# Optimization experiments

Measured on AMD Instinct MI355X. Metric: run time of the kernel, lower is better.

The kernel has to match this reference:

```python
import jax, jax.numpy as jnp
import numpy as np
import math

V, D, L, FF, H, DH, W, DM, T, B = 32000, 1024, 4, 4096, 16, 64, 256, 64, 1024, 1


def rms_norm(x, w):
    return x * jax.lax.rsqrt(jnp.mean(x * x, axis=-1, keepdims=True) + 1e-6) * w


def setup_inputs() -> dict:
    key = jax.random.key(0)
    ks = jax.random.split(key, 16)
    s = 0.02
    return {
        "x": jax.random.randint(ks[0], (B, T), 0, V),
        "embed": jax.random.normal(ks[1], (V, D), jnp.float32) * s,
        "ln_in_w": jnp.ones((D,), jnp.float32),
        "ln1_w": jnp.ones((L, D), jnp.float32),
        "lnd_w": jnp.ones((L, D), jnp.float32),
        "qkv_w": jax.random.normal(ks[2], (L, 3 * H * DH, D), jnp.float32) * s,
        "swa_out_w": jax.random.normal(ks[3], (L, D, H * DH), jnp.float32) * s,
        "k_w": jax.random.normal(ks[4], (L, H * DM, D), jnp.float32) * s,
        "v_w": jax.random.normal(ks[5], (L, H * DM, D), jnp.float32) * s,
        "q_w": jax.random.normal(ks[6], (L, H * DM, D), jnp.float32) * s,
        "beta_w": jax.random.normal(ks[7], (L, H, D), jnp.float32) * s,
        "mem_out_w": jax.random.normal(ks[8], (L, D, H * DM), jnp.float32) * s,
        "gate_w": jax.random.normal(ks[9], (L, D, D), jnp.float32) * s,
        "comb_w": jax.random.normal(ks[10], (L, D, D), jnp.float32) * s,
        "ln2_w": jnp.ones((L, D), jnp.float32),
        "wg": jax.random.normal(ks[11], (L, FF, D), jnp.float32) * s,
        "wu": jax.random.normal(ks[12], (L, FF, D), jnp.float32) * s,
        "wo": jax.random.normal(ks[13], (L, D, FF), jnp.float32) * s,
        "ln_out_w": jnp.ones((D,), jnp.float32),
    }


def _swa(h1, qkv_w, out_w):
    # h1: [B,T,D]
    qkv = jnp.einsum('btd,ed->bte', h1, qkv_w)  # [B,T,3*H*DH]
    q, k, v = jnp.split(qkv, 3, axis=-1)
    q = q.reshape(h1.shape[0], T, H, DH).transpose(0, 2, 1, 3)
    k = k.reshape(h1.shape[0], T, H, DH).transpose(0, 2, 1, 3)
    v = v.reshape(h1.shape[0], T, H, DH).transpose(0, 2, 1, 3)
    scores = jnp.einsum('bhqd,bhkd->bhqk', q, k) * (DH ** -0.5)
    pos = jnp.arange(T)
    dist = pos[:, None] - pos[None, :]
    allowed = (dist >= 0) & (dist < W)  # causal sliding window
    scores = jnp.where(allowed[None, None], scores, -jnp.inf)
    attn = jax.nn.softmax(scores, axis=-1)
    out = jnp.einsum('bhqk,bhkd->bhqd', attn, v)
    out = out.transpose(0, 2, 1, 3).reshape(h1.shape[0], T, H * DH)
    return jnp.einsum('bte,de->btd', out, out_w)


def _delta(h2, k_w, v_w, q_w, beta_w, mem_out_w):
    Bv = h2.shape[0]
    proj = lambda w: jnp.einsum('btd,ed->bte', h2, w).reshape(Bv, T, H, DM).transpose(0, 2, 1, 3)
    keys, values, queries = proj(k_w), proj(v_w), proj(q_w)
    beta = jax.nn.sigmoid(jnp.einsum('btd,hd->bht', h2, beta_w))  # [B,H,T]
    keys = keys / jnp.maximum(jnp.linalg.norm(keys, axis=-1, keepdims=True), 1e-12)
    queries = queries / jnp.maximum(jnp.linalg.norm(queries, axis=-1, keepdims=True), 1e-12)
    log_retain = jnp.log(1.0 - beta + 1e-8)
    cum_log = jnp.cumsum(log_retain, axis=-1)  # [B,H,T]
    log_decay = cum_log[..., :, None] - cum_log[..., None, :]  # [B,H,T,T]
    causal = jnp.triu(jnp.ones((T, T), dtype=bool))  # matches torch.triu mask in source
    decay = jnp.exp(jnp.minimum(log_decay, 0.0)) * causal
    kq = jnp.einsum('bhid,bhjd->bhij', queries, keys) / math.sqrt(DM)
    weights = kq * decay
    out = jnp.einsum('bhij,bhjd->bhid', weights, values)
    out = out + beta[..., None] * values
    out = out.transpose(0, 2, 1, 3).reshape(Bv, T, H * DM)
    return jnp.einsum('bte,de->btd', out, mem_out_w)


def reference(x, embed, ln_in_w, ln1_w, lnd_w, qkv_w, swa_out_w, k_w, v_w, q_w,
              beta_w, mem_out_w, gate_w, comb_w, ln2_w, wg, wu, wo, ln_out_w):
    h = rms_norm(embed[x], ln_in_w)  # [B,T,D]
    for l in range(L):
        h1 = rms_norm(h, ln1_w[l])
        h2 = rms_norm(h, lnd_w[l])
        local = _swa(h1, qkv_w[l], swa_out_w[l])
        global_ctx = _delta(h2, k_w[l], v_w[l], q_w[l], beta_w[l], mem_out_w[l])
        gate = jax.nn.sigmoid(jnp.einsum('btd,ed->bte', h1, gate_w[l]))
        mixed = jnp.einsum('btd,ed->bte', gate * local + (1.0 - gate) * global_ctx, comb_w[l])
        h = h + mixed
        hn = rms_norm(h, ln2_w[l])
        ffn = jnp.einsum('btf,df->btd', jax.nn.silu(jnp.einsum('btd,fd->btf', hn, wg[l])) * jnp.einsum('btd,fd->btf', hn, wu[l]), wo[l])
        h = h + ffn
    logits = jnp.einsum('btd,vd->btv', rms_norm(h, ln_out_w), embed)  # tied head
    return logits
```

## Files before the change

### kernel.cpp

```cpp
#include <hip/hip_runtime.h>

typedef unsigned short u16;
typedef unsigned int   u32;
typedef __attribute__((ext_vector_type(8))) __bf16 bfv8;
typedef __attribute__((ext_vector_type(4))) float  f32x4;

__device__ __forceinline__ u16 f2bf(float f){
  u32 u = __builtin_bit_cast(u32, f);
  return (u16)((u + 0x7FFFu + ((u >> 16) & 1u)) >> 16);
}
__device__ __forceinline__ float bf2f(u16 b){
  return __builtin_bit_cast(float, ((u32)b) << 16);
}
__device__ __forceinline__ u32 pk2(float a, float b){
  return (u32)f2bf(a) | ((u32)f2bf(b) << 16);
}
__device__ __forceinline__ float wsum(float v){
  #pragma unroll
  for (int m = 32; m > 0; m >>= 1) v += __shfl_xor(v, m, 64);
  return v;
}
__device__ __forceinline__ void gload16(const void* g, void* l){
  __builtin_amdgcn_global_load_lds((const __attribute__((address_space(1))) void*)g,
                                   (__attribute__((address_space(3))) void*)l, 16, 0, 0);
}

struct CBatch { const float* s[12]; long long p4[13]; u16* dst; };
__global__ __launch_bounds__(256) void flm_conv(CBatch cb)
{
  const int seg = blockIdx.y;
  const long long base = cb.p4[seg];
  const long long n4 = cb.p4[seg + 1] - base;
  const float* __restrict__ src = cb.s[seg];
  uint2* __restrict__ dst = (uint2*)cb.dst + base;
  for (long long i = (long long)blockIdx.x * 256 + threadIdx.x; i < n4;
       i += (long long)gridDim.x * 256){
    float4 v = ((const float4*)src)[i];
    uint2 p; p.x = pk2(v.x, v.y); p.y = pk2(v.z, v.w);
    dst[i] = p;
  }
}

struct GDesc {
  const u16* A; const float* Bw; float* Cf; u16* Cb;
  int lda, ldb, ldc, kbeg, kend, blk0, epi, pad;
};
struct GBatch { GDesc d[6]; int ng, total; };

template<bool BW>
__global__ __launch_bounds__(512) void flm_mgemm(GBatch gb)
{
  constexpr int LDK = BW ? 64 : 72;
  __shared__ u16 sA[128][LDK];
  __shared__ u16 sB[128][LDK];
  const int tid = threadIdx.x, lane = tid & 63, w = tid >> 6;

  const int T = gb.total, bid = blockIdx.x;
  const int q8 = T >> 3, r8 = T & 7, xc = bid & 7, of = bid >> 3;
  const int lin = (xc < r8 ? xc * (q8 + 1) : r8 * (q8 + 1) + (xc - r8) * q8) + of;
  int di = 0;
  #pragma unroll
  for (int i = 1; i < 6; i++) if (i < gb.ng && lin >= gb.d[i].blk0) di = i;
  const GDesc g = gb.d[di];
  const int local = lin - g.blk0;
  const int row0 = (local & 7) * 128;
  const int col0 = (local >> 3) * 128;
  const int wr = (w >> 2) * 64, wc = (w & 3) * 32;

  f32x4 acc[4][2];
  #pragma unroll
  for (int m = 0; m < 4; m++)
    #pragma unroll
    for (int n = 0; n < 2; n++)
      acc[m][n] = (f32x4){0.f, 0.f, 0.f, 0.f};

  const int csw = ((lane & 7) ^ (lane >> 3)) * 8;
  const u16* B16 = (const u16*)g.Bw;

  for (int k0 = g.kbeg; k0 < g.kend; k0 += 64){
    if constexpr (BW){
      const u16* a0 = g.A + (size_t)(row0 + w*16 + (lane>>3)) * g.lda + k0 + csw;
      const u16* b0 = B16 + (size_t)(col0 + w*16 + (lane>>3)) * g.ldb + k0 + csw;
      gload16(a0,                     &sA[w*16    ][0]);
      gload16(a0 + (size_t)8*g.lda,   &sA[w*16 + 8][0]);
      gload16(b0,                     &sB[w*16    ][0]);
      gload16(b0 + (size_t)8*g.ldb,   &sB[w*16 + 8][0]);
    } else {
      #pragma unroll
      for (int i = 0; i < 2; i++){
        int idx = tid + i * 512;
        int r = idx >> 3, c = (idx & 7) * 8;
        *(uint4*)&sA[r][c] = *(const uint4*)(g.A + (size_t)(row0 + r) * g.lda + k0 + c);
      }
      #pragma unroll
      for (int i = 0; i < 4; i++){
        int idx = tid + i * 512;
        int r = idx >> 4, c = (idx & 15) * 4;
        float4 v = *(const float4*)(g.Bw + (size_t)(col0 + r) * g.ldb + k0 + c);
        uint2 p; p.x = pk2(v.x, v.y); p.y = pk2(v.z, v.w);
        *(uint2*)&sB[r][c] = p;
      }
    }
    __syncthreads();
    #pragma unroll
    for (int kk = 0; kk < 2; kk++){
      bfv8 af[4], bfr[2];
      #pragma unroll
      for (int m = 0; m < 4; m++){
        int row = wr + m*16 + (lane & 15);
        if constexpr (BW){
          int slot = (kk*4 + (lane >> 4)) ^ (row & 7);
          af[m] = *(const bfv8*)((const char*)sA + row*128 + slot*16);
        } else {
          af[m] = *(const bfv8*)&sA[row][kk*32 + (lane >> 4) * 8];
        }
      }
      #pragma unroll
      for (int n = 0; n < 2; n++){
        int row = wc + n*16 + (lane & 15);
        if constexpr (BW){
          int slot = (kk*4 + (lane >> 4)) ^ (row & 7);
          bfr[n] = *(const bfv8*)((const char*)sB + row*128 + slot*16);
        } else {
          bfr[n] = *(const bfv8*)&sB[row][kk*32 + (lane >> 4) * 8];
        }
      }
      #pragma unroll
      for (int m = 0; m < 4; m++)
        #pragma unroll
        for (int n = 0; n < 2; n++)
          acc[m][n] = __builtin_amdgcn_mfma_f32_16x16x32_bf16(af[m], bfr[n], acc[m][n], 0, 0, 0);
    }
    __syncthreads();
  }

  #pragma unroll
  for (int m = 0; m < 4; m++){
    int rbase = row0 + wr + m*16 + (lane >> 4) * 4;
    #pragma unroll
    for (int n = 0; n < 2; n++){
      int col = col0 + wc + n*16 + (lane & 15);
      #pragma unroll
      for (int j = 0; j < 4; j++){
        float v = acc[m][n][j];
        size_t o = (size_t)(rbase + j) * g.ldc + col;
        switch (g.epi){
          case 0: g.Cf[o] = v; break;
          case 1: g.Cb[o] = f2bf(v); break;
          default: atomicAdd(&g.Cf[o], v); break;
        }
      }
    }
  }
}

__global__ __launch_bounds__(256) void flm_mix(
    const float* __restrict__ gr, const float* __restrict__ lo,
    const float* __restrict__ gl, u16* __restrict__ o)
{
  int i = blockIdx.x * 256 + threadIdx.x;
  float4 gv = ((const float4*)gr)[i];
  float4 lv = ((const float4*)lo)[i];
  float4 bv = ((const float4*)gl)[i];
  float sx = 1.f/(1.f+expf(-gv.x)), sy = 1.f/(1.f+expf(-gv.y));
  float sz = 1.f/(1.f+expf(-gv.z)), sw = 1.f/(1.f+expf(-gv.w));
  uint2 p;
  p.x = pk2(sx*lv.x + (1.f-sx)*bv.x, sy*lv.y + (1.f-sy)*bv.y);
  p.y = pk2(sz*lv.z + (1.f-sz)*bv.z, sw*lv.w + (1.f-sw)*bv.w);
  ((uint2*)o)[i] = p;
}

__global__ __launch_bounds__(256) void flm_silu(
    const u16* __restrict__ gg, const u16* __restrict__ uu, u16* __restrict__ o)
{
  int i = blockIdx.x * 256 + threadIdx.x;
  uint2 gv = ((const uint2*)gg)[i];
  uint2 uv = ((const uint2*)uu)[i];
  float g0 = bf2f((u16)gv.x), g1 = bf2f((u16)(gv.x >> 16));
  float g2 = bf2f((u16)gv.y), g3 = bf2f((u16)(gv.y >> 16));
  float u0 = bf2f((u16)uv.x), u1 = bf2f((u16)(uv.x >> 16));
  float u2 = bf2f((u16)uv.y), u3 = bf2f((u16)(uv.y >> 16));
  float a = g0 / (1.f + expf(-g0)) * u0;
  float b = g1 / (1.f + expf(-g1)) * u1;
  float c = g2 / (1.f + expf(-g2)) * u2;
  float d = g3 / (1.f + expf(-g3)) * u3;
  uint2 p; p.x = pk2(a, b); p.y = pk2(c, d);
  ((uint2*)o)[i] = p;
}

__global__ __launch_bounds__(256) void flm_embed(
    const int* __restrict__ x, const float* __restrict__ embed,
    const float* __restrict__ w, float* __restrict__ h)
{
  int t = blockIdx.x, tid = threadIdx.x;
  int tok = x[t];
  float4 v = ((const float4*)(embed + (size_t)tok * 1024))[tid];
  float ss = v.x*v.x + v.y*v.y + v.z*v.z + v.w*v.w;
  ss = wsum(ss);
  __shared__ float red[4];
  if ((tid & 63) == 0) red[tid >> 6] = ss;
  __syncthreads();
  float inv = rsqrtf((red[0]+red[1]+red[2]+red[3]) * (1.f/1024.f) + 1e-6f);
  float4 wv = ((const float4*)w)[tid];
  float4 o; o.x = v.x*inv*wv.x; o.y = v.y*inv*wv.y; o.z = v.z*inv*wv.z; o.w = v.w*inv*wv.w;
  ((float4*)(h + (size_t)t * 1024))[tid] = o;
}

__global__ __launch_bounds__(256) void flm_rms(
    const float* __restrict__ h, const float* __restrict__ w1, const float* __restrict__ w2,
    u16* __restrict__ o1, u16* __restrict__ o2)
{
  int t = blockIdx.x, tid = threadIdx.x;
  float4 v = ((const float4*)(h + (size_t)t * 1024))[tid];
  float ss = v.x*v.x + v.y*v.y + v.z*v.z + v.w*v.w;
  ss = wsum(ss);
  __shared__ float red[4];
  if ((tid & 63) == 0) red[tid >> 6] = ss;
  __syncthreads();
  float inv = rsqrtf((red[0]+red[1]+red[2]+red[3]) * (1.f/1024.f) + 1e-6f);
  {
    float4 wv = ((const float4*)w1)[tid];
    uint2 p; p.x = pk2(v.x*inv*wv.x, v.y*inv*wv.y); p.y = pk2(v.z*inv*wv.z, v.w*inv*wv.w);
    ((uint2*)(o1 + (size_t)t * 1024))[tid] = p;
  }
  if (o2 != nullptr){
    float4 wv = ((const float4*)w2)[tid];
    uint2 p; p.x = pk2(v.x*inv*wv.x, v.y*inv*wv.y); p.y = pk2(v.z*inv*wv.z, v.w*inv*wv.w);
    ((uint2*)(o2 + (size_t)t * 1024))[tid] = p;
  }
}

__global__ __launch_bounds__(64) void flm_betanorm(
    const u16* __restrict__ h2, const float* __restrict__ bw, float* __restrict__ beta,
    u16* __restrict__ keys, u16* __restrict__ queries)
{
  int t = blockIdx.x, lane = threadIdx.x;
  float hv[16];
  #pragma unroll
  for (int i = 0; i < 16; i++) hv[i] = bf2f(h2[(size_t)t*1024 + i*64 + lane]);
  for (int h = 0; h < 16; h++){
    float p = 0.f;
    #pragma unroll
    for (int i = 0; i < 16; i++) p += hv[i] * bw[h*1024 + i*64 + lane];
    p = wsum(p);
    if (lane == 0) beta[t*16 + h] = 1.f / (1.f + expf(-p));
  }
  #pragma unroll
  for (int h = 0; h < 16; h++){
    size_t idx = (size_t)t * 1024 + h * 64 + lane;
    float v = bf2f(keys[idx]);
    float nrm = fmaxf(sqrtf(wsum(v * v)), 1e-12f);
    keys[idx] = f2bf(v / nrm);
    float q = bf2f(queries[idx]);
    float qn = fmaxf(sqrtf(wsum(q * q)), 1e-12f);
    queries[idx] = f2bf(q / qn);
  }
}

__global__ __launch_bounds__(256) void flm_attn(
    const u16* __restrict__ qkv,
    const u16* __restrict__ keys, const u16* __restrict__ values, const u16* __restrict__ queries,
    const float* __restrict__ beta, u16* __restrict__ aout, u16* __restrict__ dout)
{
  __shared__ u16 sK[64][72];
  __shared__ u16 sVt[64][72];
  __shared__ u16 sP[4][16][72];
  const int tid = threadIdx.x, lane = tid & 63, w = tid >> 6;
  const int qt = blockIdx.x, h = blockIdx.y;
  const int base = h * 64;
  const int ri = w*16 + (lane>>4)*4;

  if (blockIdx.z == 0){
    bfv8 aq[2];
    {
      int qrow = qt*64 + w*16 + (lane & 15);
      #pragma unroll
      for (int kk = 0; kk < 2; kk++)
        aq[kk] = *(const bfv8*)(qkv + (size_t)qrow*3072 + base + kk*32 + (lane>>4)*8);
    }
    f32x4 acc_o[4];
    float m_r[4], l_r[4];
    #pragma unroll
    for (int n = 0; n < 4; n++) acc_o[n] = (f32x4){0.f,0.f,0.f,0.f};
    #pragma unroll
    for (int r = 0; r < 4; r++){ m_r[r] = -1e30f; l_r[r] = 0.f; }
    const int jt0 = (qt >= 4) ? qt - 4 : 0;

    for (int jt = qt; jt >= jt0; jt--){
      #pragma unroll
      for (int i = 0; i < 2; i++){
        int idx = tid + i*256;
        int r = idx >> 3, c = (idx & 7) * 8;
        uint4 kv = *(const uint4*)(qkv + (size_t)(jt*64+r)*3072 + 1024 + base + c);
        *(uint4*)&sK[r][c] = kv;
        uint4 vv = *(const uint4*)(qkv + (size_t)(jt*64+r)*3072 + 2048 + base + c);
        u16 tmp[8]; *(uint4*)tmp = vv;
        #pragma unroll
        for (int e = 0; e < 8; e++) sVt[c+e][r] = tmp[e];
      }
      __syncthreads();

      f32x4 sv[4];
      #pragma unroll
      for (int n = 0; n < 4; n++) sv[n] = (f32x4){0.f,0.f,0.f,0.f};
      #pragma unroll
      for (int kk = 0; kk < 2; kk++){
        #pragma unroll
        for (int n = 0; n < 4; n++){
          bfv8 bk = *(const bfv8*)&sK[n*16 + (lane & 15)][(lane>>4)*8 + kk*32];
          sv[n] = __builtin_amdgcn_mfma_f32_16x16x32_bf16(aq[kk], bk, sv[n], 0, 0, 0);
        }
      }
      #pragma unroll
      for (int n = 0; n < 4; n++){
        int cj = n*16 + (lane & 15);
        #pragma unroll
        for (int r = 0; r < 4; r++){
          float s = sv[n][r] * 0.125f;
          if (jt == qt)      { if (cj > ri + r) s = -1e30f; }
          else if (jt == jt0 && qt - jt0 == 4) { if (cj <= ri + r) s = -1e30f; }
          sv[n][r] = s;
        }
      }
      float pv[4][4], scl[4];
      #pragma unroll
      for (int r = 0; r < 4; r++){
        float mx = -1e30f;
        #pragma unroll
        for (int n = 0; n < 4; n++) mx = fmaxf(mx, sv[n][r]);
        #pragma unroll
        for (int m = 1; m < 16; m <<= 1) mx = fmaxf(mx, __shfl_xor(mx, m, 64));
        float mn = fmaxf(m_r[r], mx);
        float sc = expf(m_r[r] - mn);
        m_r[r] = mn; scl[r] = sc;
        float rs = 0.f;
        #pragma unroll
        for (int n = 0; n < 4; n++){ float p = expf(sv[n][r] - mn); pv[n][r] = p; rs += p; }
        #pragma unroll
        for (int m = 1; m < 16; m <<= 1) rs += __shfl_xor(rs, m, 64);
        l_r[r] = l_r[r] * sc + rs;
      }
      #pragma unroll
      for (int n = 0; n < 4; n++){
        #pragma unroll
        for (int r = 0; r < 4; r++){
          acc_o[n][r] *= scl[r];
          sP[w][(lane>>4)*4 + r][n*16 + (lane & 15)] = f2bf(pv[n][r]);
        }
      }
      #pragma unroll
      for (int kk = 0; kk < 2; kk++){
        bfv8 ap = *(const bfv8*)&sP[w][lane & 15][(lane>>4)*8 + kk*32];
        #pragma unroll
        for (int n = 0; n < 4; n++){
          bfv8 bv = *(const bfv8*)&sVt[n*16 + (lane & 15)][(lane>>4)*8 + kk*32];
          acc_o[n] = __builtin_amdgcn_mfma_f32_16x16x32_bf16(ap, bv, acc_o[n], 0, 0, 0);
        }
      }
      __syncthreads();
    }

    #pragma unroll
    for (int n = 0; n < 4; n++){
      int col = base + n*16 + (lane & 15);
      #pragma unroll
      for (int r = 0; r < 4; r++){
        int row = qt*64 + ri + r;
        aout[(size_t)row*1024 + col] = f2bf(acc_o[n][r] / l_r[r]);
      }
    }
  } else {
    bfv8 aq[2];
    {
      int qrow = qt*64 + w*16 + (lane & 15);
      #pragma unroll
      for (int kk = 0; kk < 2; kk++)
        aq[kk] = *(const bfv8*)(queries + (size_t)qrow*1024 + base + kk*32 + (lane>>4)*8);
    }
    f32x4 acc_o[4];
    #pragma unroll
    for (int n = 0; n < 4; n++) acc_o[n] = (f32x4){0.f,0.f,0.f,0.f};

    for (int jt = qt; jt < 16; jt++){
      #pragma unroll
      for (int i = 0; i < 2; i++){
        int idx = tid + i*256;
        int r = idx >> 3, c = (idx & 7) * 8;
        uint4 kv = *(const uint4*)(keys + (size_t)(jt*64+r)*1024 + base + c);
        *(uint4*)&sK[r][c] = kv;
        uint4 vv = *(const uint4*)(values + (size_t)(jt*64+r)*1024 + base + c);
        u16 tmp[8]; *(uint4*)tmp = vv;
        #pragma unroll
        for (int e = 0; e < 8; e++) sVt[c+e][r] = tmp[e];
      }
      __syncthreads();

      f32x4 sv[4];
      #pragma unroll
      for (int n = 0; n < 4; n++) sv[n] = (f32x4){0.f,0.f,0.f,0.f};
      #pragma unroll
      for (int kk = 0; kk < 2; kk++){
        #pragma unroll
        for (int n = 0; n < 4; n++){
          bfv8 bk = *(const bfv8*)&sK[n*16 + (lane & 15)][(lane>>4)*8 + kk*32];
          sv[n] = __builtin_amdgcn_mfma_f32_16x16x32_bf16(aq[kk], bk, sv[n], 0, 0, 0);
        }
      }
      #pragma unroll
      for (int n = 0; n < 4; n++){
        int cj = n*16 + (lane & 15);
        #pragma unroll
        for (int r = 0; r < 4; r++){
          float p = sv[n][r] * 0.125f;
          if (jt == qt && cj < ri + r) p = 0.f;
          sP[w][(lane>>4)*4 + r][n*16 + (lane & 15)] = f2bf(p);
        }
      }
      #pragma unroll
      for (int kk = 0; kk < 2; kk++){
        bfv8 ap = *(const bfv8*)&sP[w][lane & 15][(lane>>4)*8 + kk*32];
        #pragma unroll
        for (int n = 0; n < 4; n++){
          bfv8 bv = *(const bfv8*)&sVt[n*16 + (lane & 15)][(lane>>4)*8 + kk*32];
          acc_o[n] = __builtin_amdgcn_mfma_f32_16x16x32_bf16(ap, bv, acc_o[n], 0, 0, 0);
        }
      }
      __syncthreads();
    }

    #pragma unroll
    for (int n = 0; n < 4; n++){
      int col = base + n*16 + (lane & 15);
      #pragma unroll
      for (int r = 0; r < 4; r++){
        int row = qt*64 + ri + r;
        float b = beta[row*16 + h];
        float v = bf2f(values[(size_t)row*1024 + col]);
        dout[(size_t)row*1024 + col] = f2bf(acc_o[n][r] + b * v);
      }
    }
  }
}

static GDesc mkd(const u16* A, int lda, const float* Bw, int ldb,
                 float* Cf, u16* Cb, int ldc,
                 int kbeg, int kend, int blk0, int epi){
  GDesc d; d.A=A; d.Bw=Bw; d.Cf=Cf; d.Cb=Cb;
  d.lda=lda; d.ldb=ldb; d.ldc=ldc; d.kbeg=kbeg; d.kend=kend; d.blk0=blk0; d.epi=epi; d.pad=0;
  return d;
}

extern "C" void kernel_launch(void* const* d_in, const int* in_sizes, int n_in,
                              void* d_out, int out_size, void* d_ws, size_t ws_size,
                              hipStream_t stream)
{
  (void)in_sizes; (void)n_in; (void)out_size;
  const int*   x        = (const int*)d_in[0];
  const float* embed    = (const float*)d_in[1];
  const float* ln_in_w  = (const float*)d_in[2];
  const float* ln1_w    = (const float*)d_in[3];
  const float* lnd_w    = (const float*)d_in[4];
  const float* qkv_w    = (const float*)d_in[5];
  const float* swa_out_w= (const float*)d_in[6];
  const float* k_w      = (const float*)d_in[7];
  const float* v_w      = (const float*)d_in[8];
  const float* q_w      = (const float*)d_in[9];
  const float* beta_w   = (const float*)d_in[10];
  const float* mem_out_w= (const float*)d_in[11];
  const float* gate_w   = (const float*)d_in[12];
  const float* comb_w   = (const float*)d_in[13];
  const float* ln2_w    = (const float*)d_in[14];
  const float* wg       = (const float*)d_in[15];
  const float* wu       = (const float*)d_in[16];
  const float* wo       = (const float*)d_in[17];
  const float* ln_out_w = (const float*)d_in[18];
  float* out = (float*)d_out;

  char* ws = (char*)d_ws;
  const size_t KB = 1024, MB = 1u << 20;
  float* h       = (float*)(ws + 0);
  u16*   h1      = (u16*)  (ws + 4*MB);
  u16*   h2      = (u16*)  (ws + 6*MB);
  u16*   qkvb    = (u16*)  (ws + 8*MB);
  u16*   keys    = (u16*)  (ws + 14*MB);
  u16*   values  = (u16*)  (ws + 16*MB);
  u16*   queries = (u16*)  (ws + 18*MB);
  float* beta    = (float*)(ws + 20*MB);
  u16*   attn    = (u16*)  (ws + 20*MB + 256*KB);
  u16*   delt    = (u16*)  (ws + 22*MB + 256*KB);
  float* localb  = (float*)(ws + 24*MB + 256*KB);
  float* globb   = (float*)(ws + 28*MB + 256*KB);
  u16*   mcomb   = (u16*)  (ws + 32*MB + 256*KB);
  u16*   hn      = (u16*)  (ws + 36*MB);
  float* gbuf    = (float*)(ws + 40*MB);
  u16*   g16     = (u16*)  (ws + 4*MB);
  u16*   u16b    = (u16*)  (ws + 12*MB);
  u16*   sbuf    = (u16*)  (ws + 36*MB);

  u16* wb = (u16*)(ws + 44*MB);
  size_t off = 0; auto nx = [&](size_t n){ size_t o = off; off += n; return o; };
  const size_t nEmb = 32768000ULL, nQkv = 12582912ULL, nSq = 4194304ULL, nFf = 16777216ULL;
  u16* wemb  = wb + nx(nEmb);
  u16* wqkv  = wb + nx(nQkv);
  u16* wswa  = wb + nx(nSq);
  u16* wk    = wb + nx(nSq);
  u16* wv    = wb + nx(nSq);
  u16* wq    = wb + nx(nSq);
  u16* wmem  = wb + nx(nSq);
  u16* wgate = wb + nx(nSq);
  u16* wcomb = wb + nx(nSq);
  u16* wwg   = wb + nx(nFf);
  u16* wwu   = wb + nx(nFf);
  u16* wwo   = wb + nx(nFf);
  const size_t NEED = 44*MB + off * 2;
  const bool bw = (ws_size >= NEED);

  auto MG = [&](int nblk, GBatch& gbv){
    if (bw) flm_mgemm<true><<<nblk, 512, 0, stream>>>(gbv);
    else    flm_mgemm<false><<<nblk, 512, 0, stream>>>(gbv);
  };

  if (bw){
    CBatch cb;
    const float* srcs[12] = {embed, qkv_w, swa_out_w, k_w, v_w, q_w,
                             mem_out_w, gate_w, comb_w, wg, wu, wo};
    const size_t ns[12] = {nEmb, nQkv, nSq, nSq, nSq, nSq, nSq, nSq, nSq, nFf, nFf, nFf};
    long long acc4 = 0;
    for (int i = 0; i < 12; i++){ cb.s[i] = srcs[i]; cb.p4[i] = acc4; acc4 += (long long)(ns[i] >> 2); }
    cb.p4[12] = acc4; cb.dst = wb;
    flm_conv<<<dim3(1024, 12), 256, 0, stream>>>(cb);
  }

  flm_embed<<<1024, 256, 0, stream>>>(x, embed, ln_in_w, h);

  for (int l = 0; l < 4; l++){
    const size_t lq = (size_t)l * 3145728, ls = (size_t)l * 1048576, lf = (size_t)l * 4194304;
    const float* Wqkv  = bw ? (const float*)(wqkv  + lq) : qkv_w     + lq;
    const float* Wk    = bw ? (const float*)(wk    + ls) : k_w       + ls;
    const float* Wv    = bw ? (const float*)(wv    + ls) : v_w       + ls;
    const float* Wq    = bw ? (const float*)(wq    + ls) : q_w       + ls;
    const float* Wswa  = bw ? (const float*)(wswa  + ls) : swa_out_w + ls;
    const float* Wmem  = bw ? (const float*)(wmem  + ls) : mem_out_w + ls;
    const float* Wgate = bw ? (const float*)(wgate + ls) : gate_w    + ls;
    const float* Wcomb = bw ? (const float*)(wcomb + ls) : comb_w    + ls;
    const float* Wwg   = bw ? (const float*)(wwg   + lf) : wg        + lf;
    const float* Wwu   = bw ? (const float*)(wwu   + lf) : wu        + lf;
    const float* Wwo   = bw ? (const float*)(wwo   + lf) : wo        + lf;

    flm_rms<<<1024, 256, 0, stream>>>(h, ln1_w + l*1024, lnd_w + l*1024, h1, h2);

    {
      GBatch gb;
      gb.d[0] = mkd(h1, 1024, Wqkv, 1024, nullptr, qkvb, 3072, 0, 1024, 0, 1);
      gb.d[1] = mkd(h2, 1024, Wk, 1024, nullptr, keys, 1024, 0, 1024, 192, 1);
      gb.d[2] = mkd(h2, 1024, Wv, 1024, nullptr, values, 1024, 0, 1024, 256, 1);
      gb.d[3] = mkd(h2, 1024, Wq, 1024, nullptr, queries, 1024, 0, 1024, 320, 1);
      gb.d[4] = mkd(h1, 1024, Wgate, 1024, gbuf, nullptr, 1024, 0, 1024, 384, 0);
      gb.d[5] = gb.d[4]; gb.d[5].blk0 = 0x7fffffff;
      gb.ng = 5; gb.total = 448;
      MG(448, gb);
    }
    flm_betanorm<<<1024, 64, 0, stream>>>(h2, beta_w + (size_t)l*16*1024, beta, keys, queries);
    flm_attn<<<dim3(16, 16, 2), 256, 0, stream>>>(qkvb, keys, values, queries, beta, attn, delt);

    {
      GBatch gb;
      gb.d[0] = mkd(attn, 1024, Wswa, 1024, localb, nullptr, 1024, 0, 1024, 0, 0);
      gb.d[1] = mkd(delt, 1024, Wmem, 1024, globb, nullptr, 1024, 0, 1024, 64, 0);
      gb.d[2] = gb.d[1]; gb.d[2].blk0 = 0x7fffffff;
      gb.d[3] = gb.d[2]; gb.d[4] = gb.d[2]; gb.d[5] = gb.d[2];
      gb.ng = 2; gb.total = 128;
      MG(128, gb);
    }
    flm_mix<<<1024, 256, 0, stream>>>(gbuf, localb, globb, mcomb);
    {
      GBatch gb;
      gb.d[0] = mkd(mcomb, 1024, Wcomb, 1024, h, nullptr, 1024, 0, 512, 0, 5);
      gb.d[1] = mkd(mcomb, 1024, Wcomb, 1024, h, nullptr, 1024, 512, 1024, 64, 5);
      gb.d[2] = gb.d[1]; gb.d[2].blk0 = 0x7fffffff;
      gb.d[3] = gb.d[2]; gb.d[4] = gb.d[2]; gb.d[5] = gb.d[2];
      gb.ng = 2; gb.total = 128;
      MG(128, gb);
    }
    flm_rms<<<1024, 256, 0, stream>>>(h, ln2_w + l*1024, nullptr, hn, nullptr);
    {
      GBatch gb;
      gb.d[0] = mkd(hn, 1024, Wwg, 1024, nullptr, g16, 4096, 0, 1024, 0, 1);
      gb.d[1] = mkd(hn, 1024, Wwu, 1024, nullptr, u16b, 4096, 0, 1024, 256, 1);
      gb.d[2] = gb.d[1]; gb.d[2].blk0 = 0x7fffffff;
      gb.d[3] = gb.d[2]; gb.d[4] = gb.d[2]; gb.d[5] = gb.d[2];
      gb.ng = 2; gb.total = 512;
      MG(512, gb);
    }
    flm_silu<<<4096, 256, 0, stream>>>(g16, u16b, sbuf);
    {
      GBatch gb;
      for (int s = 0; s < 4; s++)
        gb.d[s] = mkd(sbuf, 4096, Wwo, 4096, h, nullptr, 1024, s*1024, (s+1)*1024, s*64, 5);
      gb.d[4] = gb.d[3]; gb.d[4].blk0 = 0x7fffffff;
      gb.d[5] = gb.d[4];
      gb.ng = 4; gb.total = 256;
      MG(256, gb);
    }
  }

  flm_rms<<<1024, 256, 0, stream>>>(h, ln_out_w, nullptr, hn, nullptr);
  {
    GBatch gb;
    gb.d[0] = mkd(hn, 1024, bw ? (const float*)wemb : embed, 1024, out, nullptr, 32000,
                  0, 1024, 0, 0);
    gb.d[1] = gb.d[0]; gb.d[1].blk0 = 0x7fffffff;
    gb.d[2] = gb.d[1]; gb.d[3] = gb.d[1]; gb.d[4] = gb.d[1]; gb.d[5] = gb.d[1];
    gb.ng = 1; gb.total = 2000;
    MG(2000, gb);
  }
}
```

Measured before the change: 1.007 ms.

## Balance delta-attention blocks by pairing query tiles and widen weight conversion

The delta branch of the attention kernel now pairs query tile p with 15-p inside one block, so each of 8 blocks per head handles a roughly equal number of key tiles. This replaces 16 blocks with triangular, uneven work, and the grid becomes 24x16. The weight conversion kernel now handles 8 floats per thread using nontemporal loads and stores, so the one-time stream does not pollute the cache. Workspace buffers are repacked to shrink the required footprint, which may let the bf16 weight path be used with a smaller workspace. The cost is fewer, longer delta blocks running serially.

```diff
diff --git a/kernel.cpp b/kernel.cpp
--- a/kernel.cpp
+++ b/kernel.cpp
@@ -4,6 +4,7 @@
 typedef unsigned int   u32;
 typedef __attribute__((ext_vector_type(8))) __bf16 bfv8;
 typedef __attribute__((ext_vector_type(4))) float  f32x4;
+typedef __attribute__((ext_vector_type(4))) u32    u32x4;
 
 __device__ __forceinline__ u16 f2bf(float f){
   u32 u = __builtin_bit_cast(u32, f);
@@ -30,14 +31,17 @@
 {
   const int seg = blockIdx.y;
   const long long base = cb.p4[seg];
-  const long long n4 = cb.p4[seg + 1] - base;
-  const float* __restrict__ src = cb.s[seg];
-  uint2* __restrict__ dst = (uint2*)cb.dst + base;
-  for (long long i = (long long)blockIdx.x * 256 + threadIdx.x; i < n4;
+  const long long n8 = (cb.p4[seg + 1] - base) >> 1;
+  const f32x4* __restrict__ src = (const f32x4*)cb.s[seg];
+  u32x4* __restrict__ dst = (u32x4*)cb.dst + (base >> 1);
+  for (long long i = (long long)blockIdx.x * 256 + threadIdx.x; i < n8;
        i += (long long)gridDim.x * 256){
-    float4 v = ((const float4*)src)[i];
-    uint2 p; p.x = pk2(v.x, v.y); p.y = pk2(v.z, v.w);
-    dst[i] = p;
+    f32x4 v0 = __builtin_nontemporal_load(src + 2*i);
+    f32x4 v1 = __builtin_nontemporal_load(src + 2*i + 1);
+    u32x4 p;
+    p.x = pk2(v0.x, v0.y); p.y = pk2(v0.z, v0.w);
+    p.z = pk2(v1.x, v1.y); p.w = pk2(v1.z, v1.w);
+    __builtin_nontemporal_store(p, dst + i);
   }
 }
 
@@ -266,11 +270,12 @@
   __shared__ u16 sVt[64][72];
   __shared__ u16 sP[4][16][72];
   const int tid = threadIdx.x, lane = tid & 63, w = tid >> 6;
-  const int qt = blockIdx.x, h = blockIdx.y;
+  const int bx = blockIdx.x, h = blockIdx.y;
   const int base = h * 64;
   const int ri = w*16 + (lane>>4)*4;
 
-  if (blockIdx.z == 0){
+  if (bx < 16){
+    const int qt = bx;
     bfv8 aq[2];
     {
       int qrow = qt*64 + w*16 + (lane & 15);
@@ -370,73 +375,78 @@
       }
     }
   } else {
-    bfv8 aq[2];
-    {
-      int qrow = qt*64 + w*16 + (lane & 15);
-      #pragma unroll
-      for (int kk = 0; kk < 2; kk++)
-        aq[kk] = *(const bfv8*)(queries + (size_t)qrow*1024 + base + kk*32 + (lane>>4)*8);
-    }
-    f32x4 acc_o[4];
-    #pragma unroll
-    for (int n = 0; n < 4; n++) acc_o[n] = (f32x4){0.f,0.f,0.f,0.f};
-
-    for (int jt = qt; jt < 16; jt++){
-      #pragma unroll
-      for (int i = 0; i < 2; i++){
-        int idx = tid + i*256;
-        int r = idx >> 3, c = (idx & 7) * 8;
-        uint4 kv = *(const uint4*)(keys + (size_t)(jt*64+r)*1024 + base + c);
-        *(uint4*)&sK[r][c] = kv;
-        uint4 vv = *(const uint4*)(values + (size_t)(jt*64+r)*1024 + base + c);
-        u16 tmp[8]; *(uint4*)tmp = vv;
-        #pragma unroll
-        for (int e = 0; e < 8; e++) sVt[c+e][r] = tmp[e];
-      }
-      __syncthreads();
-
-      f32x4 sv[4];
-      #pragma unroll
-      for (int n = 0; n < 4; n++) sv[n] = (f32x4){0.f,0.f,0.f,0.f};
-      #pragma unroll
-      for (int kk = 0; kk < 2; kk++){
+    const int p = bx - 16;
+    #pragma unroll 1
+    for (int sel = 0; sel < 2; sel++){
+      const int qt = sel ? (15 - p) : p;
+      bfv8 aq[2];
+      {
+        int qrow = qt*64 + w*16 + (lane & 15);
+        #pragma unroll
+        for (int kk = 0; kk < 2; kk++)
+          aq[kk] = *(const bfv8*)(queries + (size_t)qrow*1024 + base + kk*32 + (lane>>4)*8);
+      }
+      f32x4 acc_o[4];
+      #pragma unroll
+      for (int n = 0; n < 4; n++) acc_o[n] = (f32x4){0.f,0.f,0.f,0.f};
+
+      for (int jt = qt; jt < 16; jt++){
+        #pragma unroll
+        for (int i = 0; i < 2; i++){
+          int idx = tid + i*256;
+          int r = idx >> 3, c = (idx & 7) * 8;
+          uint4 kv = *(const uint4*)(keys + (size_t)(jt*64+r)*1024 + base + c);
+          *(uint4*)&sK[r][c] = kv;
+          uint4 vv = *(const uint4*)(values + (size_t)(jt*64+r)*1024 + base + c);
+          u16 tmp[8]; *(uint4*)tmp = vv;
+          #pragma unroll
+          for (int e = 0; e < 8; e++) sVt[c+e][r] = tmp[e];
+        }
+        __syncthreads();
+
+        f32x4 sv[4];
+        #pragma unroll
+        for (int n = 0; n < 4; n++) sv[n] = (f32x4){0.f,0.f,0.f,0.f};
+        #pragma unroll
+        for (int kk = 0; kk < 2; kk++){
+          #pragma unroll
+          for (int n = 0; n < 4; n++){
+            bfv8 bk = *(const bfv8*)&sK[n*16 + (lane & 15)][(lane>>4)*8 + kk*32];
+            sv[n] = __builtin_amdgcn_mfma_f32_16x16x32_bf16(aq[kk], bk, sv[n], 0, 0, 0);
+          }
+        }
         #pragma unroll
         for (int n = 0; n < 4; n++){
-          bfv8 bk = *(const bfv8*)&sK[n*16 + (lane & 15)][(lane>>4)*8 + kk*32];
-          sv[n] = __builtin_amdgcn_mfma_f32_16x16x32_bf16(aq[kk], bk, sv[n], 0, 0, 0);
-        }
-      }
+          int cj = n*16 + (lane & 15);
+          #pragma unroll
+          for (int r = 0; r < 4; r++){
+            float pp = sv[n][r] * 0.125f;
+            if (jt == qt && cj < ri + r) pp = 0.f;
+            sP[w][(lane>>4)*4 + r][n*16 + (lane & 15)] = f2bf(pp);
+          }
+        }
+        #pragma unroll
+        for (int kk = 0; kk < 2; kk++){
+          bfv8 ap = *(const bfv8*)&sP[w][lane & 15][(lane>>4)*8 + kk*32];
+          #pragma unroll
+          for (int n = 0; n < 4; n++){
+            bfv8 bv = *(const bfv8*)&sVt[n*16 + (lane & 15)][(lane>>4)*8 + kk*32];
+            acc_o[n] = __builtin_amdgcn_mfma_f32_16x16x32_bf16(ap, bv, acc_o[n], 0, 0, 0);
+          }
+        }
+        __syncthreads();
+      }
+
       #pragma unroll
       for (int n = 0; n < 4; n++){
-        int cj = n*16 + (lane & 15);
+        int col = base + n*16 + (lane & 15);
         #pragma unroll
         for (int r = 0; r < 4; r++){
-          float p = sv[n][r] * 0.125f;
-          if (jt == qt && cj < ri + r) p = 0.f;
-          sP[w][(lane>>4)*4 + r][n*16 + (lane & 15)] = f2bf(p);
-        }
-      }
-      #pragma unroll
-      for (int kk = 0; kk < 2; kk++){
-        bfv8 ap = *(const bfv8*)&sP[w][lane & 15][(lane>>4)*8 + kk*32];
-        #pragma unroll
-        for (int n = 0; n < 4; n++){
-          bfv8 bv = *(const bfv8*)&sVt[n*16 + (lane & 15)][(lane>>4)*8 + kk*32];
-          acc_o[n] = __builtin_amdgcn_mfma_f32_16x16x32_bf16(ap, bv, acc_o[n], 0, 0, 0);
-        }
-      }
-      __syncthreads();
-    }
-
-    #pragma unroll
-    for (int n = 0; n < 4; n++){
-      int col = base + n*16 + (lane & 15);
-      #pragma unroll
-      for (int r = 0; r < 4; r++){
-        int row = qt*64 + ri + r;
-        float b = beta[row*16 + h];
-        float v = bf2f(values[(size_t)row*1024 + col]);
-        dout[(size_t)row*1024 + col] = f2bf(acc_o[n][r] + b * v);
+          int row = qt*64 + ri + r;
+          float b = beta[row*16 + h];
+          float v = bf2f(values[(size_t)row*1024 + col]);
+          dout[(size_t)row*1024 + col] = f2bf(acc_o[n][r] + b * v);
+        }
       }
     }
   }
@@ -490,14 +500,14 @@
   u16*   delt    = (u16*)  (ws + 22*MB + 256*KB);
   float* localb  = (float*)(ws + 24*MB + 256*KB);
   float* globb   = (float*)(ws + 28*MB + 256*KB);
-  u16*   mcomb   = (u16*)  (ws + 32*MB + 256*KB);
-  u16*   hn      = (u16*)  (ws + 36*MB);
-  float* gbuf    = (float*)(ws + 40*MB);
+  float* gbuf    = (float*)(ws + 32*MB + 256*KB);
+  u16*   mcomb   = (u16*)  (ws + 36*MB + 256*KB);
+  u16*   hn      = (u16*)  (ws + 38*MB + 256*KB);
   u16*   g16     = (u16*)  (ws + 4*MB);
   u16*   u16b    = (u16*)  (ws + 12*MB);
-  u16*   sbuf    = (u16*)  (ws + 36*MB);
-
-  u16* wb = (u16*)(ws + 44*MB);
+  u16*   sbuf    = (u16*)  (ws + 20*MB);
+
+  u16* wb = (u16*)(ws + 41*MB);
   size_t off = 0; auto nx = [&](size_t n){ size_t o = off; off += n; return o; };
   const size_t nEmb = 32768000ULL, nQkv = 12582912ULL, nSq = 4194304ULL, nFf = 16777216ULL;
   u16* wemb  = wb + nx(nEmb);
@@ -512,7 +522,7 @@
   u16* wwg   = wb + nx(nFf);
   u16* wwu   = wb + nx(nFf);
   u16* wwo   = wb + nx(nFf);
-  const size_t NEED = 44*MB + off * 2;
+  const size_t NEED = 41*MB + off * 2;
   const bool bw = (ws_size >= NEED);
 
   auto MG = [&](int nblk, GBatch& gbv){
@@ -561,7 +571,7 @@
       MG(448, gb);
     }
     flm_betanorm<<<1024, 64, 0, stream>>>(h2, beta_w + (size_t)l*16*1024, beta, keys, queries);
-    flm_attn<<<dim3(16, 16, 2), 256, 0, stream>>>(qkvb, keys, values, queries, beta, attn, delt);
+    flm_attn<<<dim3(24, 16), 256, 0, stream>>>(qkvb, keys, values, queries, beta, attn, delt);
 
     {
       GBatch gb;
```

After: 1.069 ms. 1.06x slower.
